# Kernel optimization log

Hardware: AMD Instinct MI355X
Metric: run time of the kernel (lower is better)

The kernel has to match this reference:

```python
import jax, jax.numpy as jnp
import numpy as np

B, T, C, H = 16, 512, 256, 8
HS_T = C // H   # temporal head size = 32
HS_S = T // H   # spatial head size = 64
EPS = 1e-6


def _ln(x, w, b):
    m = x.mean(-1, keepdims=True)
    v = ((x - m) ** 2).mean(-1, keepdims=True)
    return (x - m) / jnp.sqrt(v + EPS) * w + b


def setup_inputs() -> dict:
    key = jax.random.key(0)
    ks = jax.random.split(key, 16)
    rn = lambda k, s, scale: jax.random.normal(k, s, dtype=jnp.float32) * scale
    inp = {
        "x_T": rn(ks[0], (B, T, C), 1.0),
        "x_S": rn(ks[1], (B, C, T), 1.0),
        # temporal attention: per-head q/k/v projections, stacked [H, hs, C]
        "Wq_t": rn(ks[2], (H, HS_T, C), C ** -0.5),
        "Wk_t": rn(ks[3], (H, HS_T, C), C ** -0.5),
        "Wv_t": rn(ks[4], (H, HS_T, C), C ** -0.5),
        "Wo": rn(ks[5], (C, C), C ** -0.5),
        # spatial attention: per-head q/k over the time axis, stacked [H, hs_s, T]
        "Wq_s": rn(ks[6], (H, HS_S, T), T ** -0.5),
        "Wk_s": rn(ks[7], (H, HS_S, T), T ** -0.5),
        # feed-forward blocks (expansion_factor=4)
        "ff1_w1": rn(ks[8], (4 * C, C), C ** -0.5),
        "ff1_b1": jnp.zeros((4 * C,), jnp.float32),
        "ff1_w2": rn(ks[9], (C, 4 * C), (4 * C) ** -0.5),
        "ff1_b2": jnp.zeros((C,), jnp.float32),
        "ff2_w1": rn(ks[10], (4 * C, C), C ** -0.5),
        "ff2_b1": jnp.zeros((4 * C,), jnp.float32),
        "ff2_w2": rn(ks[11], (C, 4 * C), (4 * C) ** -0.5),
        "ff2_b2": jnp.zeros((C,), jnp.float32),
        # layernorm affine params
        "t_ln1_w": jnp.ones((C,), jnp.float32), "t_ln1_b": jnp.zeros((C,), jnp.float32),
        "t_ln2_w": jnp.ones((C,), jnp.float32), "t_ln2_b": jnp.zeros((C,), jnp.float32),
        "s_ln1_w": jnp.ones((T,), jnp.float32), "s_ln1_b": jnp.zeros((T,), jnp.float32),
        "fus_ln_w": jnp.ones((C,), jnp.float32), "fus_ln_b": jnp.zeros((C,), jnp.float32),
    }
    return inp


def reference(x_T, x_S, Wq_t, Wk_t, Wv_t, Wo, Wq_s, Wk_s,
              ff1_w1, ff1_b1, ff1_w2, ff1_b2, ff2_w1, ff2_b1, ff2_w2, ff2_b2,
              t_ln1_w, t_ln1_b, t_ln2_w, t_ln2_b, s_ln1_w, s_ln1_b,
              fus_ln_w, fus_ln_b):
    # ---- temporal (causal) multi-head attention ----
    h = _ln(x_T, t_ln1_w, t_ln1_b)                         # [B,T,C]
    q = jnp.einsum('btc,hdc->bhtd', h, Wq_t)
    k = jnp.einsum('btc,hdc->bhtd', h, Wk_t)
    v = jnp.einsum('btc,hdc->bhtd', h, Wv_t)
    scores = jnp.einsum('bhtd,bhsd->bhts', q, k) / jnp.sqrt(jnp.float32(HS_T))
    causal = jnp.tril(jnp.ones((T, T), dtype=bool))
    scores = jnp.where(causal, scores, -jnp.inf)
    att = jax.nn.softmax(scores, axis=-1)
    o = jnp.einsum('bhts,bhsd->bhtd', att, v)              # [B,H,T,hs]
    o = o.transpose(0, 2, 1, 3).reshape(B, T, C)           # concat heads
    attn_out = o @ Wo.T
    x = x_T + attn_out
    # FFN 1
    h2 = _ln(x, t_ln2_w, t_ln2_b)
    f = jax.nn.relu(h2 @ ff1_w1.T + ff1_b1) @ ff1_w2.T + ff1_b2
    temporal_out = x + f                                   # [B,T,C]
    # ---- spatial (non-causal) attention over neurons ----
    hs = _ln(x_S, s_ln1_w, s_ln1_b)                        # [B,C,T]
    qs = jnp.einsum('bct,hdt->bhcd', hs, Wq_s)
    ks = jnp.einsum('bct,hdt->bhcd', hs, Wk_s)
    sc = jnp.einsum('bhcd,bhed->bhce', qs, ks) / jnp.sqrt(jnp.float32(HS_S))
    spatial_weights = jax.nn.softmax(sc, axis=-1).mean(axis=1)   # [B,C,C], mean over heads
    # ---- fusion ----
    fused = jnp.einsum('bce,bte->btc', spatial_weights, temporal_out)
    x2 = temporal_out + fused
    h3 = _ln(x2, fus_ln_w, fus_ln_b)
    f2 = jax.nn.relu(h3 @ ff2_w1.T + ff2_b1) @ ff2_w2.T + ff2_b2
    out = x2 + f2
    return out, spatial_weights
```

## Files before the change

kernel.cpp:

```cpp
#include <hip/hip_runtime.h>
#include <hip/hip_bf16.h>

typedef __hip_bfloat16 bf16;
typedef __attribute__((ext_vector_type(8))) short short8;
typedef __attribute__((ext_vector_type(4))) float f32x4;

#define F_BIAS 1
#define F_RELU 2
#define F_RES  4

__device__ __forceinline__ void st_out(float* p, float v){ *p = v; }
__device__ __forceinline__ void st_out(bf16* p, float v){ *p = __float2bfloat16(v); }
__device__ __forceinline__ short f2bs(float f){
  bf16 h = __float2bfloat16(f);
  return *reinterpret_cast<short*>(&h);
}

__device__ __forceinline__ void gl_lds16(const void* g, void* l){
  __builtin_amdgcn_global_load_lds(
      (const __attribute__((address_space(1))) void*)g,
      (__attribute__((address_space(3))) void*)l, 16, 0, 0);
}

__device__ __forceinline__ void lgkm_barrier(){
  asm volatile("s_waitcnt lgkmcnt(0)" ::: "memory");
  __builtin_amdgcn_s_barrier();
}

struct ProArgs {
  const float* wsrc[10];
  bf16* wdst[10];
  const float *xT, *xS, *tl1w, *tl1b, *sl1w, *sl1b;
  bf16 *hT, *hS;
};

template<int RL>
__device__ __forceinline__ void wave_ln(bf16* __restrict__ dst,
    const float* __restrict__ src, const float* __restrict__ w,
    const float* __restrict__ bvec, int row){
  int lane = threadIdx.x & 63;
  const float* s = src + (size_t)row*RL;
  float4 v0 = *(const float4*)(s + lane*4);
  float4 v1 = {0.f,0.f,0.f,0.f};
  float sum = v0.x+v0.y+v0.z+v0.w;
  float sq  = v0.x*v0.x+v0.y*v0.y+v0.z*v0.z+v0.w*v0.w;
  if (RL == 512){
    v1 = *(const float4*)(s + 256 + lane*4);
    sum += v1.x+v1.y+v1.z+v1.w;
    sq  += v1.x*v1.x+v1.y*v1.y+v1.z*v1.z+v1.w*v1.w;
  }
  #pragma unroll
  for (int off=32; off; off>>=1){
    sum += __shfl_xor(sum, off, 64);
    sq  += __shfl_xor(sq , off, 64);
  }
  const float inv = 1.0f/(float)RL;
  float mean = sum*inv;
  float rstd = rsqrtf(sq*inv - mean*mean + 1e-6f);
  float4 w0 = *(const float4*)(w + lane*4);
  float4 b0 = *(const float4*)(bvec + lane*4);
  bf16* d = dst + (size_t)row*RL;
  short4 o;
  o.x = f2bs((v0.x-mean)*rstd*w0.x + b0.x);
  o.y = f2bs((v0.y-mean)*rstd*w0.y + b0.y);
  o.z = f2bs((v0.z-mean)*rstd*w0.z + b0.z);
  o.w = f2bs((v0.w-mean)*rstd*w0.w + b0.w);
  *(short4*)((short*)d + lane*4) = o;
  if (RL == 512){
    float4 w1 = *(const float4*)(w + 256 + lane*4);
    float4 b1 = *(const float4*)(bvec + 256 + lane*4);
    short4 o1;
    o1.x = f2bs((v1.x-mean)*rstd*w1.x + b1.x);
    o1.y = f2bs((v1.y-mean)*rstd*w1.y + b1.y);
    o1.z = f2bs((v1.z-mean)*rstd*w1.z + b1.z);
    o1.w = f2bs((v1.w-mean)*rstd*w1.w + b1.w);
    *(short4*)((short*)d + 256 + lane*4) = o1;
  }
}

__global__ __launch_bounds__(256) void prologue(ProArgs a){
  int blk = blockIdx.x;
  int wid = threadIdx.x >> 6;
  if (blk < 1792){
    int v = blk*256 + threadIdx.x;
    int e = v*4;
    int seg = (e>=65536)+(e>=131072)+(e>=196608)+(e>=262144)+(e>=524288)
            + (e>=786432)+(e>=1048576)+(e>=1310720)+(e>=1572864);
    const int starts[10] = {0,65536,131072,196608,262144,524288,786432,
                            1048576,1310720,1572864};
    int off = e - starts[seg];
    float4 f = *(const float4*)(a.wsrc[seg] + off);
    short4 o;
    o.x = f2bs(f.x); o.y = f2bs(f.y); o.z = f2bs(f.z); o.w = f2bs(f.w);
    *(short4*)((short*)a.wdst[seg] + off) = o;
  } else if (blk < 1792 + 2048){
    wave_ln<256>(a.hT, a.xT, a.tl1w, a.tl1b, (blk-1792)*4 + wid);
  } else {
    wave_ln<512>(a.hS, a.xS, a.sl1w, a.sl1b, (blk-3840)*4 + wid);
  }
}

template<int BM, int BN, int BK>
__device__ __forceinline__ void gemm_body(
    short* __restrict__ AsB, short* __restrict__ BsB,
    const bf16* __restrict__ A, const bf16* __restrict__ B,
    float* __restrict__ outF, bf16* __restrict__ outB,
    const float* __restrict__ bias, const float* __restrict__ resid,
    int K, int lda, int ldb, int ldc, int flags, int m0, int n0){
  int tid = threadIdx.x;
  int w = tid>>6, lane = tid&63, quad = lane>>4, l16 = lane&15;
  constexpr int MF  = BM/32;
  constexpr int NF  = BN/32;
  constexpr int CPR = BK/8;
  constexpr int CA  = BM*CPR/256;
  constexpr int CB  = BN*CPR/256;
  int wm = (w>>1)*(BM/2), wn = (w&1)*(BN/2);
  f32x4 acc[MF][NF];
  #pragma unroll
  for (int r=0;r<MF;r++)
    #pragma unroll
    for (int j=0;j<NF;j++)
      acc[r][j] = (f32x4){0.f,0.f,0.f,0.f};

  auto stage = [&](int k0, int half){
    short* as = AsB + half*(BM*BK);
    short* bs = BsB + half*(BN*BK);
    #pragma unroll
    for (int c=0;c<CA;c++){
      int ch = tid + c*256;
      int row = ch / CPR, p = ch % CPR;
      gl_lds16(A + (size_t)(m0+row)*lda + k0 + ((p ^ (row&(CPR-1)))*8),
               &as[row*BK + p*8]);
    }
    #pragma unroll
    for (int c=0;c<CB;c++){
      int ch = tid + c*256;
      int row = ch / CPR, p = ch % CPR;
      gl_lds16(B + (size_t)(n0+row)*ldb + k0 + ((p ^ (row&(CPR-1)))*8),
               &bs[row*BK + p*8]);
    }
  };

  stage(0, 0);
  int nk = K / BK;
  for (int t = 0; t < nk; ++t){
    __syncthreads();
    if (t+1 < nk) stage((t+1)*BK, (t+1)&1);
    const short* as = AsB + (t&1)*(BM*BK);
    const short* bs = BsB + (t&1)*(BN*BK);
    #pragma unroll
    for (int ks=0; ks<BK/32; ++ks){
      short8 af[MF], bfr[NF];
      #pragma unroll
      for (int r=0;r<MF;r++){
        int rr = wm + r*16 + l16;
        af[r] = *(short8*)&as[rr*BK + (((ks*4+quad) ^ (rr&(CPR-1)))*8)];
      }
      #pragma unroll
      for (int j=0;j<NF;j++){
        int rr = wn + j*16 + l16;
        bfr[j] = *(short8*)&bs[rr*BK + (((ks*4+quad) ^ (rr&(CPR-1)))*8)];
      }
      #pragma unroll
      for (int r=0;r<MF;r++)
        #pragma unroll
        for (int j=0;j<NF;j++)
          acc[r][j] = __builtin_amdgcn_mfma_f32_16x16x32_bf16(af[r], bfr[j], acc[r][j], 0,0,0);
    }
  }
  #pragma unroll
  for (int r=0;r<MF;r++){
    int mb = m0 + wm + r*16 + quad*4;
    #pragma unroll
    for (int j=0;j<NF;j++){
      int n = n0 + wn + j*16 + l16;
      float bv = (flags & F_BIAS) ? bias[n] : 0.0f;
      #pragma unroll
      for (int e=0;e<4;e++){
        float v = acc[r][j][e] + bv;
        if (flags & F_RELU) v = fmaxf(v, 0.0f);
        long long idx = (long long)(mb+e)*ldc + n;
        if (flags & F_RES) v += resid[idx];
        if (outF) outF[idx] = v;
        if (outB) st_out(outB + idx, v);
      }
    }
  }
}

template<int BM, int BN, int BK>
__global__ __launch_bounds__(256) void gemm_mfma(
    const bf16* __restrict__ A, const bf16* __restrict__ B,
    float* __restrict__ outF, bf16* __restrict__ outB,
    const float* __restrict__ bias, const float* __restrict__ resid,
    int K, int lda, int ldb, int ldc, int flags){
  __shared__ __align__(16) short As[2*BM*BK];
  __shared__ __align__(16) short Bs[2*BN*BK];
  gemm_body<BM,BN,BK>(As,Bs,A,B,outF,outB,bias,resid,K,lda,ldb,ldc,flags,
                      blockIdx.x*BM, blockIdx.y*BN);
}

struct GArgs {
  const bf16 *A, *B;
  float* outF; bf16* outB;
  const float *bias, *resid;
  int K, lda, ldb, ldc, flags, ty;
};
__global__ __launch_bounds__(256) void gemm_dual(GArgs g0, GArgs g1, int n0){
  __shared__ __align__(16) short As[2*64*64];
  __shared__ __align__(16) short Bs[2*128*64];
  int id = blockIdx.x;
  bool first = id < n0;
  const GArgs& g = first ? g0 : g1;
  int t = first ? id : id - n0;
  int bx = t / g.ty, by = t - bx*g.ty;
  gemm_body<64,128,64>(As, Bs, g.A, g.B, g.outF, g.outB, g.bias, g.resid,
                       g.K, g.lda, g.ldb, g.ldc, g.flags, bx*64, by*128);
}

__global__ __launch_bounds__(512) void gemm_ln(
    const bf16* __restrict__ A, const bf16* __restrict__ B,
    float* __restrict__ outF, bf16* __restrict__ outLN,
    const float* __restrict__ resid,
    const float* __restrict__ lnw, const float* __restrict__ lnb,
    int K, int lda, int ldb, int flags,
    long long sA, long long sB, long long sO, long long sR){
  int bz = blockIdx.z;
  A += (size_t)bz*sA;
  B += (size_t)bz*sB;
  long long obase = (long long)bz*sO;
  __shared__ __align__(16) short As[2*32*64];
  __shared__ __align__(16) short Bs[2*256*64];
  __shared__ float redS[4][32], redQ[4][32];
  int tid = threadIdx.x;
  int m0 = blockIdx.x*32;
  int w = tid>>6, lane = tid&63, quad = lane>>4, l16 = lane&15;
  int wm = (w>>2)*16;
  int wn = (w&3)*64;
  f32x4 acc[4];
  #pragma unroll
  for (int j=0;j<4;j++) acc[j] = (f32x4){0.f,0.f,0.f,0.f};

  auto stage = [&](int k0, int half){
    short* as = As + half*(32*64);
    short* bs = Bs + half*(256*64);
    if (tid < 256){
      int row = tid >> 3, p = tid & 7;
      gl_lds16(A + (size_t)(m0+row)*lda + k0 + ((p ^ (row&7))*8),
               &as[row*64 + p*8]);
    }
    #pragma unroll
    for (int c=0;c<4;c++){
      int ch = tid + c*512;
      int row = ch >> 3, p = ch & 7;
      gl_lds16(B + (size_t)row*ldb + k0 + ((p ^ (row&7))*8),
               &bs[row*64 + p*8]);
    }
  };

  stage(0, 0);
  int nk = K / 64;
  for (int t = 0; t < nk; ++t){
    __syncthreads();
    if (t+1 < nk) stage((t+1)*64, (t+1)&1);
    const short* as = As + (t&1)*(32*64);
    const short* bs = Bs + (t&1)*(256*64);
    #pragma unroll
    for (int ks=0; ks<2; ++ks){
      int rr = wm + l16;
      short8 af = *(short8*)&as[rr*64 + (((ks*4+quad) ^ (rr&7))*8)];
      #pragma unroll
      for (int j=0;j<4;j++){
        int rb = wn + j*16 + l16;
        short8 bfr = *(short8*)&bs[rb*64 + (((ks*4+quad) ^ (rb&7))*8)];
        acc[j] = __builtin_amdgcn_mfma_f32_16x16x32_bf16(af, bfr, acc[j], 0,0,0);
      }
    }
  }
  #pragma unroll
  for (int e=0;e<4;e++){
    int row = wm + quad*4 + e;
    float s = 0.f, q2 = 0.f;
    #pragma unroll
    for (int j=0;j<4;j++){
      float v = acc[j][e];
      if (flags & F_RES)
        v += resid[(long long)bz*sR + (long long)(m0+row)*256 + wn + j*16 + l16];
      acc[j][e] = v;
      s += v; q2 += v*v;
    }
    #pragma unroll
    for (int off=1; off<16; off<<=1){
      s  += __shfl_xor(s , off, 16);
      q2 += __shfl_xor(q2, off, 16);
    }
    if (l16==0){ redS[w&3][row] = s; redQ[w&3][row] = q2; }
  }
  __syncthreads();
  #pragma unroll
  for (int e=0;e<4;e++){
    int row = wm + quad*4 + e;
    float tot = redS[0][row] + redS[1][row] + redS[2][row] + redS[3][row];
    float tq  = redQ[0][row] + redQ[1][row] + redQ[2][row] + redQ[3][row];
    float mean = tot * (1.0f/256.0f);
    float var  = tq * (1.0f/256.0f) - mean*mean;
    float rstd = rsqrtf(var + 1e-6f);
    #pragma unroll
    for (int j=0;j<4;j++){
      int col = wn + j*16 + l16;
      float v = acc[j][e];
      long long idx = obase + (long long)(m0+row)*256 + col;
      if (outF) outF[idx] = v;
      outLN[idx] = __float2bfloat16((v-mean)*rstd*lnw[col] + lnb[col]);
    }
  }
}

__device__ __forceinline__ int fsw(int row){ return (row>>1)&3; }
__global__ __launch_bounds__(256) void flash_mfma(
    const bf16* __restrict__ qkv, bf16* __restrict__ o){
  int qt = (int)gridDim.x - 1 - (int)blockIdx.x;
  int h = blockIdx.y, b = blockIdx.z;
  int tid = threadIdx.x;
  int w = tid>>6, lane = tid&63, quad = lane>>4, l16 = lane&15;
  __shared__ __align__(16) bf16 Qs[64*32];
  __shared__ __align__(16) bf16 Ks[2][64*32];
  __shared__ __align__(16) bf16 Vt[2][32*72];
  __shared__ __align__(16) bf16 Ps[64*72];
  const bf16* base = qkv + (size_t)b*512*768;
  int t0 = qt*64;
  int srow = tid>>2, spos = tid&3;
  gl_lds16(base + (size_t)(t0+srow)*768 + h*32 + ((spos ^ fsw(srow))*8),
           &Qs[srow*32 + spos*8]);
  {
    const bf16* rp = base + (size_t)srow*768 + h*32;
    gl_lds16(rp + 256 + ((spos ^ fsw(srow))*8), &Ks[0][srow*32 + spos*8]);
    short8 v = *(const short8*)(rp + 512 + spos*8);
    #pragma unroll
    for (int q=0;q<8;q++){
      short tmp = v[q];
      Vt[0][(spos*8+q)*72 + srow] = *(bf16*)&tmp;
    }
  }
  f32x4 accO[2];
  accO[0] = (f32x4){0.f,0.f,0.f,0.f};
  accO[1] = (f32x4){0.f,0.f,0.f,0.f};
  float m_i[4], l_i[4];
  #pragma unroll
  for (int e=0;e<4;e++){ m_i[e] = -3.0e38f; l_i[e] = 0.0f; }
  const float scale = 0.17677669529663687f;
  __syncthreads();
  int rq = w*16 + l16;
  short8 aq = *(short8*)&Qs[rq*32 + ((quad ^ fsw(rq))*8)];

  for (int kt = 0; kt <= qt; ++kt){
    if (kt) __syncthreads();
    int cur = kt&1, nxt = cur^1;
    bool pre = (kt < qt);
    short8 vpre;
    if (pre){
      const bf16* rp = base + (size_t)((kt+1)*64 + srow)*768 + h*32;
      gl_lds16(rp + 256 + ((spos ^ fsw(srow))*8), &Ks[nxt][srow*32 + spos*8]);
      vpre = *(const short8*)(rp + 512 + spos*8);
    }
    f32x4 S[4];
    #pragma unroll
    for (int j2=0;j2<4;j2++){
      int rk = j2*16 + l16;
      short8 bk = *(short8*)&Ks[cur][rk*32 + ((quad ^ fsw(rk))*8)];
      S[j2] = __builtin_amdgcn_mfma_f32_16x16x32_bf16(aq, bk,
                (f32x4){0.f,0.f,0.f,0.f}, 0,0,0);
    }
    bool diag = (kt == qt);
    int s0 = kt*64;
    int qrow_base = t0 + w*16 + quad*4;
    #pragma unroll
    for (int e=0;e<4;e++){
      float sv[4];
      #pragma unroll
      for (int j2=0;j2<4;j2++){
        float x = S[j2][e]*scale;
        if (diag && (s0 + j2*16 + l16 > qrow_base + e)) x = -3.0e38f;
        sv[j2] = x;
      }
      float mx = fmaxf(fmaxf(sv[0],sv[1]), fmaxf(sv[2],sv[3]));
      #pragma unroll
      for (int off=1; off<16; off<<=1) mx = fmaxf(mx, __shfl_xor(mx, off, 64));
      float m_new = fmaxf(m_i[e], mx);
      float alpha = __expf(m_i[e]-m_new);
      float rs = 0.0f;
      #pragma unroll
      for (int j2=0;j2<4;j2++){
        float p = __expf(sv[j2]-m_new);
        rs += p;
        Ps[(w*16+quad*4+e)*72 + j2*16 + l16] = __float2bfloat16(p);
      }
      #pragma unroll
      for (int off=1; off<16; off<<=1) rs += __shfl_xor(rs, off, 64);
      l_i[e] = l_i[e]*alpha + rs;
      m_i[e] = m_new;
      accO[0][e] *= alpha;
      accO[1][e] *= alpha;
    }
    asm volatile("s_waitcnt lgkmcnt(0)" ::: "memory");
    __builtin_amdgcn_sched_barrier(0);
    #pragma unroll
    for (int sh=0; sh<2; ++sh){
      short8 ap = *(short8*)&Ps[(w*16+l16)*72 + sh*32 + quad*8];
      #pragma unroll
      for (int dh=0; dh<2; ++dh){
        short8 bv = *(short8*)&Vt[cur][(dh*16+l16)*72 + sh*32 + quad*8];
        accO[dh] = __builtin_amdgcn_mfma_f32_16x16x32_bf16(ap, bv, accO[dh], 0,0,0);
      }
    }
    if (pre){
      #pragma unroll
      for (int q=0;q<8;q++){
        short tmp = vpre[q];
        Vt[nxt][(spos*8+q)*72 + srow] = *(bf16*)&tmp;
      }
    }
  }
  #pragma unroll
  for (int e=0;e<4;e++){
    float inv = 1.0f/l_i[e];
    int t = t0 + w*16 + quad*4 + e;
    bf16* op = o + ((size_t)(b*512+t))*256 + h*32 + l16;
    op[0]  = __float2bfloat16(accO[0][e]*inv);
    op[16] = __float2bfloat16(accO[1][e]*inv);
  }
}

__device__ void spatial_body(bf16* __restrict__ Qall, bf16* __restrict__ KsB,
                             const bf16* __restrict__ qk,
                             float* __restrict__ out1, bf16* __restrict__ swB,
                             int ct, int b){
  int tid = threadIdx.x;
  int w = tid>>6, lane = tid&63, quad = lane>>4, l16 = lane&15;
  __shared__ float redM[4][16], redS2[4][16];
  const bf16* qbase = qk + ((size_t)(b*256 + ct*16))*1024;
  #pragma unroll
  for (int c=0;c<4;c++){
    int ch = tid + c*256;
    int row = ch>>6, p = ch&63;
    gl_lds16(qbase + (size_t)row*1024 + ((p ^ (row&7))*8), &Qall[row*512 + p*8]);
  }
  auto stageK = [&](int ck, int half){
    bf16* ks = KsB + half*(128*64);
    int h = ck>>1, hf = ck&1;
    #pragma unroll
    for (int c=0;c<4;c++){
      int ch = tid + c*256;
      int el = ch>>3, p = ch&7;
      int e  = hf*128 + el;
      gl_lds16(qk + ((size_t)(b*256 + e))*1024 + 512 + h*64 + ((p ^ (el&7))*8),
               &ks[el*64 + p*8]);
    }
  };
  stageK(0, 0);
  float fRes[4][4];
  #pragma unroll
  for (int f=0;f<4;f++)
    #pragma unroll
    for (int e=0;e<4;e++) fRes[f][e] = 0.0f;
  f32x4 acc[4];

  for (int ck=0; ck<16; ++ck){
    int h = ck>>1, hf = ck&1;
    __syncthreads();
    if (ck+1 < 16) stageK(ck+1, (ck+1)&1);
    const bf16* kcur = KsB + (ck&1)*(128*64);
    if (hf == 0){
      #pragma unroll
      for (int f=0;f<4;f++) acc[f] = (f32x4){0.f,0.f,0.f,0.f};
    }
    #pragma unroll
    for (int ki=0; ki<2; ++ki){
      int g = h*8 + ki*4 + quad;
      short8 aq = *(short8*)&Qall[l16*512 + ((g ^ (l16&7))*8)];
      #pragma unroll
      for (int j=0;j<2;j++){
        int el = w*32 + j*16 + l16;
        short8 bk = *(short8*)&kcur[el*64 + (((ki*4+quad) ^ (el&7))*8)];
        acc[hf*2+j] = __builtin_amdgcn_mfma_f32_16x16x32_bf16(aq, bk, acc[hf*2+j], 0,0,0);
      }
    }
    if (hf == 1){
      #pragma unroll
      for (int e=0;e<4;e++){
        float m = -3.0e38f;
        #pragma unroll
        for (int f=0;f<4;f++){
          float s = acc[f][e]*0.125f;
          acc[f][e] = s;
          m = fmaxf(m, s);
        }
        #pragma unroll
        for (int off=1; off<16; off<<=1) m = fmaxf(m, __shfl_xor(m, off, 16));
        if (l16==0) redM[w][quad*4+e] = m;
      }
      lgkm_barrier();
      #pragma unroll
      for (int e=0;e<4;e++){
        int r = quad*4+e;
        float m = fmaxf(fmaxf(redM[0][r],redM[1][r]), fmaxf(redM[2][r],redM[3][r]));
        float s = 0.0f;
        #pragma unroll
        for (int f=0;f<4;f++){
          float p = __expf(acc[f][e]-m);
          acc[f][e] = p; s += p;
        }
        #pragma unroll
        for (int off=1; off<16; off<<=1) s += __shfl_xor(s, off, 16);
        if (l16==0) redS2[w][r] = s;
      }
      lgkm_barrier();
      #pragma unroll
      for (int e=0;e<4;e++){
        int r = quad*4+e;
        float tot = redS2[0][r]+redS2[1][r]+redS2[2][r]+redS2[3][r];
        float inv = 0.125f/tot;
        #pragma unroll
        for (int f=0;f<4;f++) fRes[f][e] += acc[f][e]*inv;
      }
    }
  }
  #pragma unroll
  for (int e=0;e<4;e++){
    int c = ct*16 + quad*4 + e;
    size_t rb = ((size_t)b*256 + c)*256;
    #pragma unroll
    for (int f=0;f<4;f++){
      int col = (f>>1)*128 + w*32 + (f&1)*16 + l16;
      out1[rb+col] = fRes[f][e];
      swB[rb+col]  = __float2bfloat16(fRes[f][e]);
    }
  }
}

__global__ __launch_bounds__(256) void mixed_l2(
    const bf16* __restrict__ gA, const bf16* __restrict__ gB,
    float* __restrict__ gOutF, bf16* __restrict__ gOutB,
    const float* __restrict__ gBias, const float* __restrict__ gResid,
    const bf16* __restrict__ qk, float* __restrict__ out1,
    bf16* __restrict__ swB){
  __shared__ __align__(16) short lds[24576];
  int id = blockIdx.x;
  if (id < 256){
    int bx = id >> 1, by = id & 1;
    gemm_body<64,128,64>(lds, lds + 2*64*64, gA, gB, gOutF, gOutB, gBias, gResid,
                         1024, 1024, 1024, 256, F_BIAS|F_RES, bx*64, by*128);
  } else {
    int t = id - 256;
    spatial_body((bf16*)lds, (bf16*)(lds + 8192), qk, out1, swB, t & 15, t >> 4);
  }
}

extern "C" void kernel_launch(void* const* d_in, const int* in_sizes, int n_in,
                              void* d_out, int out_size, void* d_ws, size_t ws_size,
                              hipStream_t stream){
  (void)in_sizes; (void)n_in; (void)out_size; (void)ws_size;
  const float* x_T  = (const float*)d_in[0];
  const float* x_S  = (const float*)d_in[1];
  const float* Wq_t = (const float*)d_in[2];
  const float* Wk_t = (const float*)d_in[3];
  const float* Wv_t = (const float*)d_in[4];
  const float* Wo   = (const float*)d_in[5];
  const float* Wq_s = (const float*)d_in[6];
  const float* Wk_s = (const float*)d_in[7];
  const float* f1w1 = (const float*)d_in[8];
  const float* f1b1 = (const float*)d_in[9];
  const float* f1w2 = (const float*)d_in[10];
  const float* f1b2 = (const float*)d_in[11];
  const float* f2w1 = (const float*)d_in[12];
  const float* f2b1 = (const float*)d_in[13];
  const float* f2w2 = (const float*)d_in[14];
  const float* f2b2 = (const float*)d_in[15];
  const float* tl1w = (const float*)d_in[16];
  const float* tl1b = (const float*)d_in[17];
  const float* tl2w = (const float*)d_in[18];
  const float* tl2b = (const float*)d_in[19];
  const float* sl1w = (const float*)d_in[20];
  const float* sl1b = (const float*)d_in[21];
  const float* flw  = (const float*)d_in[22];
  const float* flb  = (const float*)d_in[23];

  float* ws = (float*)d_ws;
  size_t off = 0;
  bf16*  Wqkvb  = (bf16*)(ws + off); off += 768*256/2;
  bf16*  Wob    = (bf16*)(ws + off); off += 256*256/2;
  bf16*  f1w1b  = (bf16*)(ws + off); off += 1024*256/2;
  bf16*  f1w2b  = (bf16*)(ws + off); off += 256*1024/2;
  bf16*  f2w1b  = (bf16*)(ws + off); off += 1024*256/2;
  bf16*  f2w2b  = (bf16*)(ws + off); off += 256*1024/2;
  bf16*  WSb    = (bf16*)(ws + off); off += 1024*512/2;
  bf16*  bufHb  = (bf16*)(ws + off); off += (size_t)8192*256/2;
  bf16*  bufHSb = (bf16*)(ws + off); off += (size_t)4096*512/2;
  bf16*  bufQKVb= (bf16*)(ws + off); off += (size_t)8192*768/2;
  bf16*  bufBigB= (bf16*)(ws + off); off += (size_t)8192*1024/2;
  bf16*  bufOb  = (bf16*)(ws + off); off += (size_t)8192*256/2;
  bf16*  bufTOb = (bf16*)(ws + off); off += (size_t)8192*256/2;
  bf16*  swB    = (bf16*)(ws + off); off += (size_t)16*256*256/2;
  bf16*  qkB    = (bf16*)(ws + off); off += (size_t)4096*1024/2;
  float* bufX   = ws + off; off += (size_t)8192*256;
  float* bufTO  = ws + off; off += (size_t)8192*256;
  float* bufX2  = ws + off; off += (size_t)8192*256;

  float* out0 = (float*)d_out;
  float* out1 = out0 + (size_t)16*512*256;

  ProArgs pa;
  pa.wsrc[0]=Wq_t;  pa.wdst[0]=Wqkvb;
  pa.wsrc[1]=Wk_t;  pa.wdst[1]=Wqkvb+65536;
  pa.wsrc[2]=Wv_t;  pa.wdst[2]=Wqkvb+131072;
  pa.wsrc[3]=Wo;    pa.wdst[3]=Wob;
  pa.wsrc[4]=f1w1;  pa.wdst[4]=f1w1b;
  pa.wsrc[5]=f1w2;  pa.wdst[5]=f1w2b;
  pa.wsrc[6]=f2w1;  pa.wdst[6]=f2w1b;
  pa.wsrc[7]=f2w2;  pa.wdst[7]=f2w2b;
  pa.wsrc[8]=Wq_s;  pa.wdst[8]=WSb;
  pa.wsrc[9]=Wk_s;  pa.wdst[9]=WSb+262144;
  pa.xT=x_T; pa.xS=x_S; pa.tl1w=tl1w; pa.tl1b=tl1b;
  pa.sl1w=sl1w; pa.sl1b=sl1b; pa.hT=bufHb; pa.hS=bufHSb;
  prologue<<<4864,256,0,stream>>>(pa);

  GArgs gq, gs;
  gq.A=bufHb;  gq.B=Wqkvb; gq.outF=nullptr; gq.outB=bufQKVb;
  gq.bias=nullptr; gq.resid=nullptr;
  gq.K=256; gq.lda=256; gq.ldb=256; gq.ldc=768; gq.flags=0; gq.ty=6;
  gs.A=bufHSb; gs.B=WSb;   gs.outF=nullptr; gs.outB=qkB;
  gs.bias=nullptr; gs.resid=nullptr;
  gs.K=512; gs.lda=512; gs.ldb=512; gs.ldc=1024; gs.flags=0; gs.ty=8;
  gemm_dual<<<1280,256,0,stream>>>(gq, gs, 768);

  flash_mfma<<<dim3(8,8,16),256,0,stream>>>(bufQKVb, bufOb);
  gemm_ln<<<dim3(256,1,1),512,0,stream>>>(bufOb, Wob, bufX, bufHb,
        x_T, tl2w, tl2b, 256, 256,256, F_RES, 0,0,0,0);
  gemm_mfma<64,128,64><<<dim3(128,8),256,0,stream>>>(bufHb, f1w1b, nullptr, bufBigB,
        f1b1, nullptr, 256, 256,256,1024, F_BIAS|F_RELU);
  mixed_l2<<<512,256,0,stream>>>(bufBigB, f1w2b, bufTO, bufTOb, f1b2, bufX,
        qkB, out1, swB);
  gemm_ln<<<dim3(16,1,16),512,0,stream>>>(bufTOb, swB, bufX2, bufHb,
        bufTO, flw, flb, 256, 256,256, F_RES,
        131072, 65536, 131072, 131072);
  gemm_mfma<64,128,64><<<dim3(128,8),256,0,stream>>>(bufHb, f2w1b, nullptr, bufBigB,
        f2b1, nullptr, 256, 256,256,1024, F_BIAS|F_RELU);
  gemm_mfma<64,128,64><<<dim3(128,2),256,0,stream>>>(bufBigB, f2w2b, out0, nullptr,
        f2b2, bufX2, 1024, 1024,1024,256, F_BIAS|F_RES);
}
```

Before: 308.0 us.

## Split spatial attention into its own kernel and stage full-head K tiles

Moves the spatial attention softmax out of the mixed FFN2/spatial kernel into a standalone kernel launched right after the QKV projection. The FFN1 second GEMM now runs as a plain gemm_mfma launch. The spatial kernel now stages all 256 key rows per head at once in a larger double-buffered LDS area and does one softmax pass per head instead of two half passes. This halves the loop trips and the barriers per head, but uses about 80KB of LDS per block, which lowers occupancy. It also gives up the overlap that came from co-scheduling the spatial work with the GEMM in one launch.

```diff
diff --git a/kernel.cpp b/kernel.cpp
--- a/kernel.cpp
+++ b/kernel.cpp
@@ -431,12 +431,14 @@
   }
 }
 
-__device__ void spatial_body(bf16* __restrict__ Qall, bf16* __restrict__ KsB,
-                             const bf16* __restrict__ qk,
-                             float* __restrict__ out1, bf16* __restrict__ swB,
-                             int ct, int b){
+__global__ __launch_bounds__(256) void spatial_fused(
+    const bf16* __restrict__ qk, float* __restrict__ out1,
+    bf16* __restrict__ swB){
+  int ct = blockIdx.x & 15, b = blockIdx.x >> 4;
   int tid = threadIdx.x;
   int w = tid>>6, lane = tid&63, quad = lane>>4, l16 = lane&15;
+  __shared__ __align__(16) bf16 Qall[16*512];
+  __shared__ __align__(16) bf16 Ks[2][256*64];
   __shared__ float redM[4][16], redS2[4][16];
   const bf16* qbase = qk + ((size_t)(b*256 + ct*16))*1024;
   #pragma unroll
@@ -445,84 +447,77 @@
     int row = ch>>6, p = ch&63;
     gl_lds16(qbase + (size_t)row*1024 + ((p ^ (row&7))*8), &Qall[row*512 + p*8]);
   }
-  auto stageK = [&](int ck, int half){
-    bf16* ks = KsB + half*(128*64);
-    int h = ck>>1, hf = ck&1;
-    #pragma unroll
-    for (int c=0;c<4;c++){
+  auto stageK = [&](int h, int half){
+    bf16* ks = Ks[half];
+    #pragma unroll
+    for (int c=0;c<8;c++){
       int ch = tid + c*256;
-      int el = ch>>3, p = ch&7;
-      int e  = hf*128 + el;
-      gl_lds16(qk + ((size_t)(b*256 + e))*1024 + 512 + h*64 + ((p ^ (el&7))*8),
-               &ks[el*64 + p*8]);
+      int e = ch>>3, p = ch&7;
+      gl_lds16(qk + ((size_t)(b*256 + e))*1024 + 512 + h*64 + ((p ^ (e&7))*8),
+               &ks[e*64 + p*8]);
     }
   };
   stageK(0, 0);
   float fRes[4][4];
   #pragma unroll
-  for (int f=0;f<4;f++)
-    #pragma unroll
-    for (int e=0;e<4;e++) fRes[f][e] = 0.0f;
-  f32x4 acc[4];
-
-  for (int ck=0; ck<16; ++ck){
-    int h = ck>>1, hf = ck&1;
+  for (int j=0;j<4;j++)
+    #pragma unroll
+    for (int e=0;e<4;e++) fRes[j][e] = 0.0f;
+
+  for (int h=0; h<8; ++h){
     __syncthreads();
-    if (ck+1 < 16) stageK(ck+1, (ck+1)&1);
-    const bf16* kcur = KsB + (ck&1)*(128*64);
-    if (hf == 0){
-      #pragma unroll
-      for (int f=0;f<4;f++) acc[f] = (f32x4){0.f,0.f,0.f,0.f};
-    }
+    if (h+1 < 8) stageK(h+1, (h+1)&1);
+    const bf16* kcur = Ks[h&1];
+    f32x4 acc[4];
+    #pragma unroll
+    for (int j=0;j<4;j++) acc[j] = (f32x4){0.f,0.f,0.f,0.f};
     #pragma unroll
     for (int ki=0; ki<2; ++ki){
       int g = h*8 + ki*4 + quad;
       short8 aq = *(short8*)&Qall[l16*512 + ((g ^ (l16&7))*8)];
       #pragma unroll
-      for (int j=0;j<2;j++){
-        int el = w*32 + j*16 + l16;
-        short8 bk = *(short8*)&kcur[el*64 + (((ki*4+quad) ^ (el&7))*8)];
-        acc[hf*2+j] = __builtin_amdgcn_mfma_f32_16x16x32_bf16(aq, bk, acc[hf*2+j], 0,0,0);
-      }
-    }
-    if (hf == 1){
-      #pragma unroll
-      for (int e=0;e<4;e++){
-        float m = -3.0e38f;
-        #pragma unroll
-        for (int f=0;f<4;f++){
-          float s = acc[f][e]*0.125f;
-          acc[f][e] = s;
-          m = fmaxf(m, s);
-        }
-        #pragma unroll
-        for (int off=1; off<16; off<<=1) m = fmaxf(m, __shfl_xor(m, off, 16));
-        if (l16==0) redM[w][quad*4+e] = m;
-      }
-      lgkm_barrier();
-      #pragma unroll
-      for (int e=0;e<4;e++){
-        int r = quad*4+e;
-        float m = fmaxf(fmaxf(redM[0][r],redM[1][r]), fmaxf(redM[2][r],redM[3][r]));
-        float s = 0.0f;
-        #pragma unroll
-        for (int f=0;f<4;f++){
-          float p = __expf(acc[f][e]-m);
-          acc[f][e] = p; s += p;
-        }
-        #pragma unroll
-        for (int off=1; off<16; off<<=1) s += __shfl_xor(s, off, 16);
-        if (l16==0) redS2[w][r] = s;
-      }
-      lgkm_barrier();
-      #pragma unroll
-      for (int e=0;e<4;e++){
-        int r = quad*4+e;
-        float tot = redS2[0][r]+redS2[1][r]+redS2[2][r]+redS2[3][r];
-        float inv = 0.125f/tot;
-        #pragma unroll
-        for (int f=0;f<4;f++) fRes[f][e] += acc[f][e]*inv;
-      }
+      for (int j=0;j<4;j++){
+        int e = w*64 + j*16 + l16;
+        short8 bk = *(short8*)&kcur[e*64 + (((ki*4+quad) ^ (e&7))*8)];
+        acc[j] = __builtin_amdgcn_mfma_f32_16x16x32_bf16(aq, bk, acc[j], 0,0,0);
+      }
+    }
+    #pragma unroll
+    for (int e=0;e<4;e++){
+      float m = -3.0e38f;
+      #pragma unroll
+      for (int j=0;j<4;j++){
+        float s = acc[j][e]*0.125f;
+        acc[j][e] = s;
+        m = fmaxf(m, s);
+      }
+      #pragma unroll
+      for (int off=1; off<16; off<<=1) m = fmaxf(m, __shfl_xor(m, off, 16));
+      if (l16==0) redM[w][quad*4+e] = m;
+    }
+    lgkm_barrier();
+    #pragma unroll
+    for (int e=0;e<4;e++){
+      int r = quad*4+e;
+      float m = fmaxf(fmaxf(redM[0][r],redM[1][r]), fmaxf(redM[2][r],redM[3][r]));
+      float s = 0.0f;
+      #pragma unroll
+      for (int j=0;j<4;j++){
+        float p = __expf(acc[j][e]-m);
+        acc[j][e] = p; s += p;
+      }
+      #pragma unroll
+      for (int off=1; off<16; off<<=1) s += __shfl_xor(s, off, 16);
+      if (l16==0) redS2[w][r] = s;
+    }
+    lgkm_barrier();
+    #pragma unroll
+    for (int e=0;e<4;e++){
+      int r = quad*4+e;
+      float tot = redS2[0][r]+redS2[1][r]+redS2[2][r]+redS2[3][r];
+      float inv = 0.125f/tot;
+      #pragma unroll
+      for (int j=0;j<4;j++) fRes[j][e] += acc[j][e]*inv;
     }
   }
   #pragma unroll
@@ -530,29 +525,11 @@
     int c = ct*16 + quad*4 + e;
     size_t rb = ((size_t)b*256 + c)*256;
     #pragma unroll
-    for (int f=0;f<4;f++){
-      int col = (f>>1)*128 + w*32 + (f&1)*16 + l16;
-      out1[rb+col] = fRes[f][e];
-      swB[rb+col]  = __float2bfloat16(fRes[f][e]);
-    }
-  }
-}
-
-__global__ __launch_bounds__(256) void mixed_l2(
-    const bf16* __restrict__ gA, const bf16* __restrict__ gB,
-    float* __restrict__ gOutF, bf16* __restrict__ gOutB,
-    const float* __restrict__ gBias, const float* __restrict__ gResid,
-    const bf16* __restrict__ qk, float* __restrict__ out1,
-    bf16* __restrict__ swB){
-  __shared__ __align__(16) short lds[24576];
-  int id = blockIdx.x;
-  if (id < 256){
-    int bx = id >> 1, by = id & 1;
-    gemm_body<64,128,64>(lds, lds + 2*64*64, gA, gB, gOutF, gOutB, gBias, gResid,
-                         1024, 1024, 1024, 256, F_BIAS|F_RES, bx*64, by*128);
-  } else {
-    int t = id - 256;
-    spatial_body((bf16*)lds, (bf16*)(lds + 8192), qk, out1, swB, t & 15, t >> 4);
+    for (int j=0;j<4;j++){
+      int col = w*64 + j*16 + l16;
+      out1[rb+col] = fRes[j][e];
+      swB[rb+col]  = __float2bfloat16(fRes[j][e]);
+    }
   }
 }
 
@@ -633,13 +610,15 @@
   gs.K=512; gs.lda=512; gs.ldb=512; gs.ldc=1024; gs.flags=0; gs.ty=8;
   gemm_dual<<<1280,256,0,stream>>>(gq, gs, 768);
 
+  spatial_fused<<<256,256,0,stream>>>(qkB, out1, swB);
+
   flash_mfma<<<dim3(8,8,16),256,0,stream>>>(bufQKVb, bufOb);
   gemm_ln<<<dim3(256,1,1),512,0,stream>>>(bufOb, Wob, bufX, bufHb,
         x_T, tl2w, tl2b, 256, 256,256, F_RES, 0,0,0,0);
   gemm_mfma<64,128,64><<<dim3(128,8),256,0,stream>>>(bufHb, f1w1b, nullptr, bufBigB,
         f1b1, nullptr, 256, 256,256,1024, F_BIAS|F_RELU);
-  mixed_l2<<<512,256,0,stream>>>(bufBigB, f1w2b, bufTO, bufTOb, f1b2, bufX,
-        qkB, out1, swB);
+  gemm_mfma<64,128,64><<<dim3(128,2),256,0,stream>>>(bufBigB, f1w2b, bufTO, bufTOb,
+        f1b2, bufX, 1024, 1024,1024,256, F_BIAS|F_RES);
   gemm_ln<<<dim3(16,1,16),512,0,stream>>>(bufTOb, swB, bufX2, bufHb,
         bufTO, flw, flb, 256, 256,256, F_RES,
         131072, 65536, 131072, 131072);
```

Result: faster. 291.4 us (-5.4%).
